# Kernel optimization log

Hardware: AMD Instinct MI355X
Metric: run time of the kernel (lower is better)

Reference implementation:

```python
import jax, jax.numpy as jnp
import numpy as np
import math

NUM_LEAD = 12
PATCHES = 100  # patch_num_v * patch_num_h = 5 * 20
HEADS = 12
HID = 768
DH = HID // HEADS  # 64
SEQ = NUM_LEAD * PATCHES + NUM_LEAD + 1  # 1213
INTER = 3072
BATCH = 8


def _layer_norm(x, g, b, eps=1e-12):
    u = x.mean(-1, keepdims=True)
    s = ((x - u) ** 2).mean(-1, keepdims=True)
    return g * (x - u) / jnp.sqrt(s + eps) + b


def _lead_mask():
    # make_mask with fusion == 0: additive bias applied to query rows [0, NUM_LEAD+1)
    cols = jnp.arange(SEQ)
    # CLS row: 1 at lead-token positions 1..NUM_LEAD
    cls_row = jnp.where((cols >= 1) & (cols < NUM_LEAD + 1), 1.0, 0.0)
    # Lead rows: 1 everywhere except own patch block
    i = jnp.arange(NUM_LEAD)[:, None]
    start = NUM_LEAD + 1 + PATCHES * i
    in_block = (cols[None, :] >= start) & (cols[None, :] < start + PATCHES)
    lead_rows = jnp.where(in_block, 0.0, 1.0)
    mask = jnp.concatenate([cls_row[None, :], lead_rows], axis=0)  # [NUM_LEAD+1, SEQ]
    return mask * (-99999.0)


def setup_inputs() -> dict:
    key = jax.random.key(0)
    ks = jax.random.split(key, 12)
    std = 0.02
    d = {
        "hidden_states": jax.random.normal(ks[0], (BATCH, SEQ, HID), jnp.float32),
        "attention_mask": jnp.zeros((BATCH, 1, 1, SEQ), jnp.float32),
        "Wq": jax.random.normal(ks[1], (HID, HID), jnp.float32) * std,
        "bq": jnp.zeros((HID,), jnp.float32),
        "Wk": jax.random.normal(ks[2], (HID, HID), jnp.float32) * std,
        "bk": jnp.zeros((HID,), jnp.float32),
        "Wv": jax.random.normal(ks[3], (HID, HID), jnp.float32) * std,
        "bv": jnp.zeros((HID,), jnp.float32),
        "Wo": jax.random.normal(ks[4], (HID, HID), jnp.float32) * std,
        "bo": jnp.zeros((HID,), jnp.float32),
        "gamma1": jnp.ones((HID,), jnp.float32),
        "beta1": jnp.zeros((HID,), jnp.float32),
        "Wi": jax.random.normal(ks[5], (HID, INTER), jnp.float32) * std,
        "bi": jnp.zeros((INTER,), jnp.float32),
        "Wd": jax.random.normal(ks[6], (INTER, HID), jnp.float32) * std,
        "bd": jnp.zeros((HID,), jnp.float32),
        "gamma2": jnp.ones((HID,), jnp.float32),
        "beta2": jnp.zeros((HID,), jnp.float32),
    }
    return d


def reference(hidden_states, attention_mask, Wq, bq, Wk, bk, Wv, bv, Wo, bo,
              gamma1, beta1, Wi, bi, Wd, bd, gamma2, beta2):
    B, S, _ = hidden_states.shape

    def heads(x):  # [B,S,HID] -> [B,H,S,DH]
        return x.reshape(B, S, HEADS, DH).transpose(0, 2, 1, 3)

    q = heads(hidden_states @ Wq + bq)
    k = heads(hidden_states @ Wk + bk)
    v = heads(hidden_states @ Wv + bv)

    scores = jnp.einsum("bhqd,bhkd->bhqk", q, k) / math.sqrt(DH)
    scores = scores + attention_mask  # broadcast [B,1,1,S]
    lead_mask = _lead_mask()  # [NUM_LEAD+1, SEQ]
    scores = scores.at[:, :, : NUM_LEAD + 1, :].add(lead_mask[None, None])

    probs = jax.nn.softmax(scores, axis=-1)  # dropout is identity in eval
    ctx = jnp.einsum("bhqk,bhkd->bhqd", probs, v)
    ctx = ctx.transpose(0, 2, 1, 3).reshape(B, S, HID)

    attn_out = _layer_norm(ctx @ Wo + bo + hidden_states, gamma1, beta1)
    inter = jax.nn.gelu(attn_out @ Wi + bi, approximate=False)  # exact erf gelu
    out = _layer_norm(inter @ Wd + bd + attn_out, gamma2, beta2)
    return out
```

## Files before the change

kernel.cpp:

```cpp
#include <hip/hip_runtime.h>
#include <hip/hip_bf16.h>
#include <stdint.h>

typedef unsigned short u16;
typedef unsigned int u32;
typedef __attribute__((ext_vector_type(8))) short frag8;
typedef __attribute__((ext_vector_type(4))) float f32x4;

#define SEQ 1213
#define SEQP 1216
#define BATCH 8
#define HEADS 12
#define DH 64
#define HID 768
#define INTER 3072
#define BS (BATCH*SEQ)
#define LOG2E 1.44269504088896f

#define MFMA(a,b,c) __builtin_amdgcn_mfma_f32_16x16x32_bf16(a,b,c,0,0,0)

__device__ __forceinline__ float b2f(u16 u){ u32 i=((u32)u)<<16; float f; __builtin_memcpy(&f,&i,4); return f; }
__device__ __forceinline__ u16 f2b(float f){ u32 i; __builtin_memcpy(&i,&f,4); i = i + 0x7fffu + ((i>>16)&1u); return (u16)(i>>16); }

__device__ __forceinline__ void async16(const u16* g, u16* l){
  __builtin_amdgcn_global_load_lds((const __attribute__((address_space(1))) u32*)(uintptr_t)g,
                                   (__attribute__((address_space(3))) u32*)(uintptr_t)l, 16, 0, 0);
}

__device__ __forceinline__ int xcd_swz(int f, int nwg){
  int cpx = nwg >> 3;
  return (f & 7)*cpx + (f >> 3);
}

__device__ __forceinline__ float gelu_exact_fast(float v){
  float y = v * 0.70710678118654752f;
  float a = fabsf(y);
  float t = __builtin_amdgcn_rcpf(fmaf(0.3275911f, a, 1.0f));
  float p = t*fmaf(t, fmaf(t, fmaf(t, fmaf(t, 1.061405429f, -1.453152027f),
                                   1.421413741f), -0.284496736f), 0.254829592f);
  float e = exp2f(a*a * -LOG2E);
  float er = fmaf(-p, e, 1.0f);
  er = copysignf(er, y);
  return 0.5f * v * (1.0f + er);
}

__global__ __launch_bounds__(256) void convert_arr(const void* __restrict__ src,
  u16* __restrict__ dst, int n8, const u16* __restrict__ probe)
{
  const bool f32 = (probe[0] == 0);
  int i = blockIdx.x*256 + threadIdx.x;
  if (i >= n8) return;
  u16 tmp[8];
  if (f32){
    const float* s = (const float*)src + (size_t)i*8;
#pragma unroll
    for (int j=0;j<8;j++) tmp[j] = f2b(s[j]);
  } else {
    *(uint4*)tmp = *((const uint4*)src + i);
  }
  *((uint4*)dst + i) = *(const uint4*)tmp;
}

__global__ __launch_bounds__(256) void convert_small(
  const void* bq, const void* bk, const void* bv, const void* bo,
  const void* bi, const void* bd, const void* g1, const void* be1,
  const void* g2, const void* be2, const void* am,
  u16* __restrict__ dst, const u16* __restrict__ probe)
{
  const int starts[12] = {0,768,1536,2304,3072,6144,6912,7680,8448,9216,9984,19688};
  const void* srcs[11] = {bq,bk,bv,bo,bi,bd,g1,be1,g2,be2,am};
  const bool f32 = (probe[0] == 0);
  int e = (blockIdx.x*256 + threadIdx.x) * 8;
  if (e >= 19688) return;
  int seg = 0;
#pragma unroll
  for (int k=1;k<11;k++) if (starts[k] <= e) seg = k;
  int off = e - starts[seg];
  const void* s = srcs[seg];
  u16 tmp[8];
  if (f32){
    const float* sf = (const float*)s + off;
#pragma unroll
    for (int j=0;j<8;j++) tmp[j] = f2b(sf[j]);
  } else {
    const u16* sh = (const u16*)s + off;
#pragma unroll
    for (int j=0;j<8;j++) tmp[j] = sh[j];
  }
  *(uint4*)(dst + e) = *(const uint4*)tmp;
}

__global__ __launch_bounds__(256) void transpose2(const void* __restrict__ in,
  u16* __restrict__ out, int R, int C, const u16* __restrict__ probe)
{
  const bool f32 = (probe[0] == 0);
  __shared__ u16 tile[32][33];
  const int bx = blockIdx.x*32, by = blockIdx.y*32;
  const int tx = threadIdx.x & 31, ty = threadIdx.x >> 5;
  if (f32){
    const float* inf_ = (const float*)in;
#pragma unroll
    for (int i=ty;i<32;i+=8) tile[i][tx] = f2b(inf_[(size_t)(by+i)*C + bx+tx]);
  } else {
    const u16* inh = (const u16*)in;
#pragma unroll
    for (int i=ty;i<32;i+=8) tile[i][tx] = inh[(size_t)(by+i)*C + bx+tx];
  }
  __syncthreads();
#pragma unroll
  for (int i=ty;i<32;i+=8) out[(size_t)(bx+i)*R + by+tx] = tile[tx][i];
}

__global__ __launch_bounds__(256) void transpose4(const void* __restrict__ w0,
  const void* __restrict__ w1, const void* __restrict__ w2, const void* __restrict__ w3,
  u16* __restrict__ dqkv, u16* __restrict__ dwo, const u16* __restrict__ probe)
{
  const bool f32 = (probe[0] == 0);
  __shared__ u16 tile[32][33];
  const int z = blockIdx.z;
  const void* in = z==0 ? w0 : (z==1 ? w1 : (z==2 ? w2 : w3));
  u16* out = (z<3) ? (dqkv + (size_t)z*768*768) : dwo;
  const int bx = blockIdx.x*32, by = blockIdx.y*32;
  const int tx = threadIdx.x & 31, ty = threadIdx.x >> 5;
  if (f32){
    const float* inf_ = (const float*)in;
#pragma unroll
    for (int i=ty;i<32;i+=8) tile[i][tx] = f2b(inf_[(size_t)(by+i)*768 + bx+tx]);
  } else {
    const u16* inh = (const u16*)in;
#pragma unroll
    for (int i=ty;i<32;i+=8) tile[i][tx] = inh[(size_t)(by+i)*768 + bx+tx];
  }
  __syncthreads();
#pragma unroll
  for (int i=ty;i<32;i+=8) out[(size_t)(bx+i)*768 + by+tx] = tile[tx][i];
}

__global__ __launch_bounds__(256) void vtrans(const u16* __restrict__ V, u16* __restrict__ VT)
{
  __shared__ u16 tile[32][33];
  const int bh = blockIdx.z;
  const int s0 = blockIdx.x*32;
  const int d0 = blockIdx.y*32;
  const int tx = threadIdx.x & 31, ty = threadIdx.x >> 5;
  const u16* Vp = V + (size_t)bh*SEQ*64;
  u16* Tp = VT + (size_t)bh*64*SEQP;
#pragma unroll
  for (int i=ty;i<32;i+=8){
    int s = s0 + i;
    tile[i][tx] = (s < SEQ) ? Vp[(size_t)s*64 + d0 + tx] : (u16)0;
  }
  __syncthreads();
#pragma unroll
  for (int i=ty;i<32;i+=8)
    Tp[(size_t)(d0 + i)*SEQP + s0 + tx] = tile[tx][i];
}

__device__ __forceinline__ void gemm_tile(
    const u16* __restrict__ A, const u16* __restrict__ BT,
    int M, int K, int m0, int n0,
    u16* ldsA, u16* ldsB, f32x4 acc[4][4])
{
  const int t = threadIdx.x;
  const int w = t >> 6, l = t & 63;
  const int lw = l & 15, lh = l >> 4;
  const int rowo = (w >> 1) << 6;
  const int colo = (w & 1) << 6;
  const int srow = w*8 + (l>>3);
  const int scol = ((l&7) ^ ((l>>3)&7)) * 8;

  const u16* gpA[4]; const u16* gpB[4];
  u16* lpA[4]; u16* lpB[4];
#pragma unroll
  for (int p=0;p<4;p++){
    int ra = m0 + p*32 + srow; if (ra >= M) ra = M-1;
    gpA[p] = A  + (size_t)ra*K + scol;
    gpB[p] = BT + (size_t)(n0 + p*32 + srow)*K + scol;
    lpA[p] = ldsA + (p*32 + w*8)*64 + l*8;
    lpB[p] = ldsB + (p*32 + w*8)*64 + l*8;
  }

  const int slot0 = lw & 7;
  for (int k0 = 0; k0 < K; k0 += 64) {
    __syncthreads();
#pragma unroll
    for (int p=0;p<4;p++) async16(gpA[p] + k0, lpA[p]);
#pragma unroll
    for (int p=0;p<4;p++) async16(gpB[p] + k0, lpB[p]);
    __syncthreads();
#pragma unroll
    for (int kk=0;kk<2;kk++){
      const int slot = ((kk*4 + lh) ^ slot0) * 8;
      frag8 af[4], bf[4];
#pragma unroll
      for (int mi=0;mi<4;mi++) af[mi] = *(const frag8*)(ldsA + (rowo + mi*16 + lw)*64 + slot);
#pragma unroll
      for (int ni=0;ni<4;ni++) bf[ni] = *(const frag8*)(ldsB + (colo + ni*16 + lw)*64 + slot);
#pragma unroll
      for (int mi=0;mi<4;mi++)
#pragma unroll
        for (int ni=0;ni<4;ni++)
          acc[mi][ni] = MFMA(af[mi], bf[ni], acc[mi][ni]);
    }
  }
}

__global__ __launch_bounds__(256,2) void gemm_qkv(
  const u16* __restrict__ A, const u16* __restrict__ BT,
  const u16* __restrict__ bq, const u16* __restrict__ bk, const u16* __restrict__ bv,
  u16* __restrict__ Qo, u16* __restrict__ Ko, u16* __restrict__ Vo)
{
  __shared__ __align__(16) u16 ldsA[128*64];
  __shared__ __align__(16) u16 ldsB[128*64];
  f32x4 acc[4][4];
#pragma unroll
  for (int i=0;i<4;i++)
#pragma unroll
    for (int j=0;j<4;j++) acc[i][j] = 0.f;
  const int m0 = blockIdx.x*128, n0 = blockIdx.y*128;
  gemm_tile(A, BT, BS, HID, m0, n0, ldsA, ldsB, acc);
  const int t=threadIdx.x, w=t>>6, l=t&63, lw=l&15, lh=l>>4;
  const int rowb = m0 + ((w>>1)<<6), colb = n0 + ((w&1)<<6);
#pragma unroll
  for (int ni=0;ni<4;ni++){
    int cc = colb + ni*16 + lw;
    int which = cc / HID;
    int n2 = cc - which*HID;
    int h = n2 >> 6, d = n2 & 63;
    const u16* bp = which==0 ? bq : (which==1 ? bk : bv);
    u16* op = which==0 ? Qo : (which==1 ? Ko : Vo);
    float bias = b2f(bp[n2]);
    float scale = which==0 ? 0.125f : 1.0f;
#pragma unroll
    for (int mi=0;mi<4;mi++){
#pragma unroll
      for (int r=0;r<4;r++){
        int rr = rowb + mi*16 + lh*4 + r;
        if (rr < BS){
          int bi_ = rr / SEQ;
          int si  = rr - bi_*SEQ;
          float v = (acc[mi][ni][r] + bias) * scale;
          op[(((size_t)(bi_*HEADS + h))*SEQ + si)*64 + d] = f2b(v);
        }
      }
    }
  }
}

__global__ __launch_bounds__(256,2) void gemm_resid(
  const u16* __restrict__ A, const u16* __restrict__ BT,
  const u16* __restrict__ bias, const u16* __restrict__ resid,
  u16* __restrict__ out, int N, int K)
{
  __shared__ __align__(16) u16 ldsA[128*64];
  __shared__ __align__(16) u16 ldsB[128*64];
  f32x4 acc[4][4];
#pragma unroll
  for (int i=0;i<4;i++)
#pragma unroll
    for (int j=0;j<4;j++) acc[i][j] = 0.f;
  const int m0 = blockIdx.x*128, n0 = blockIdx.y*128;
  gemm_tile(A, BT, BS, K, m0, n0, ldsA, ldsB, acc);
  const int t=threadIdx.x, w=t>>6, l=t&63, lw=l&15, lh=l>>4;
  const int rowb = m0 + ((w>>1)<<6), colb = n0 + ((w&1)<<6);
#pragma unroll
  for (int ni=0;ni<4;ni++){
    int cc = colb + ni*16 + lw;
    float bv_ = b2f(bias[cc]);
#pragma unroll
    for (int mi=0;mi<4;mi++){
#pragma unroll
      for (int r=0;r<4;r++){
        int rr = rowb + mi*16 + lh*4 + r;
        if (rr < BS){
          float v = acc[mi][ni][r] + bv_ + b2f(resid[(size_t)rr*N + cc]);
          out[(size_t)rr*N + cc] = f2b(v);
        }
      }
    }
  }
}

__global__ __launch_bounds__(256,2) void gemm_gelu(
  const u16* __restrict__ A, const u16* __restrict__ BT,
  const u16* __restrict__ bias, u16* __restrict__ out, int N, int K)
{
  __shared__ __align__(16) u16 ldsA[128*64];
  __shared__ __align__(16) u16 ldsB[128*64];
  f32x4 acc[4][4];
#pragma unroll
  for (int i=0;i<4;i++)
#pragma unroll
    for (int j=0;j<4;j++) acc[i][j] = 0.f;
  const int m0 = blockIdx.x*128, n0 = blockIdx.y*128;
  gemm_tile(A, BT, BS, K, m0, n0, ldsA, ldsB, acc);
  const int t=threadIdx.x, w=t>>6, l=t&63, lw=l&15, lh=l>>4;
  const int rowb = m0 + ((w>>1)<<6), colb = n0 + ((w&1)<<6);
#pragma unroll
  for (int ni=0;ni<4;ni++){
    int cc = colb + ni*16 + lw;
    float bv_ = b2f(bias[cc]);
#pragma unroll
    for (int mi=0;mi<4;mi++){
#pragma unroll
      for (int r=0;r<4;r++){
        int rr = rowb + mi*16 + lh*4 + r;
        if (rr < BS){
          float v = gelu_exact_fast(acc[mi][ni][r] + bv_);
          out[(size_t)rr*N + cc] = f2b(v);
        }
      }
    }
  }
}

__global__ __launch_bounds__(512,1) void attn_kernel(
  const u16* __restrict__ Qb, const u16* __restrict__ Kb, const u16* __restrict__ Vt,
  const u16* __restrict__ amask, u16* __restrict__ ctx)
{
  __shared__ __align__(16) u16 smem[17664];
  u16* sKb = smem;
  u16* sVb = smem + 2*64*72;
  float* sEmb = (float*)(smem + 2*64*72 + 2*64*64);
  u16* sQP = smem;

  const int t = threadIdx.x, w = t>>6, l = t&63, lw = l&15, lh = l>>4;
  int f = xcd_swz(blockIdx.y*gridDim.x + blockIdx.x, gridDim.x*gridDim.y);
  const int bh = f / gridDim.x, b = bh / HEADS;
  const int q0 = (f % gridDim.x) * 128;
  const size_t hb = (size_t)bh * SEQ * 64;
  const u16* Qp = Qb + hb;
  const u16* Kp = Kb + hb;
  const u16* Vp = Vt + (size_t)bh * 64 * SEQP;

  const int rr = t >> 3, c = t & 7;
  const int wsw = ((c ^ (rr&7))<<3);
  const int cc0 = (lw&7) ^ lh;

  {
#pragma unroll
    for (int i=0;i<2;i++){
      int qr = i*64 + rr;
      int s = q0 + qr; if (s > SEQ-1) s = SEQ-1;
      *(uint4*)(sQP + qr*72 + c*8) = *(const uint4*)(Qp + (size_t)s*64 + c*8);
    }
  }

  uint4 kreg, vreg; float emreg = 0.f;
  {
    kreg = *(const uint4*)(Kp + (size_t)rr*64 + c*8);
    vreg = *(const uint4*)(Vp + (size_t)rr*SEQP + c*8);
    if (t < 64) emreg = b2f(amask[b*SEQ + t]) * LOG2E;
  }
  __syncthreads();

  frag8 qa[2];
#pragma unroll
  for (int kk=0;kk<2;kk++) qa[kk] = *(const frag8*)(sQP + (w*16 + lw)*72 + kk*32 + lh*8);
  __syncthreads();

  *(uint4*)(sKb + rr*72 + c*8) = kreg;
  *(uint4*)(sVb + rr*64 + wsw) = vreg;
  if (t < 64) sEmb[t] = emreg;
  __syncthreads();

  union { u32 u[4]; frag8 f; } onesu;
  onesu.u[0]=onesu.u[1]=onesu.u[2]=onesu.u[3]=0x3F803F80u;
  const frag8 vones = onesu.f;

  f32x4 o[4]; f32x4 lO = 0.f;
#pragma unroll
  for (int i=0;i<4;i++) o[i] = 0.f;
  const bool leadwave = (q0 == 0) && (w == 0);

  const int nkt = (SEQ + 63) / 64;
  for (int kt = 0; kt < nkt; kt++) {
    const int p = kt & 1;
    const u16* sKp = sKb + p*64*72;
    const u16* sVp = sVb + p*64*64;
    const float* sEp = sEmb + p*64;
    const bool pf_next = (kt+1 < nkt);
    if (pf_next){
      int s = (kt+1)*64 + rr; if (s > SEQ-1) s = SEQ-1;
      kreg = *(const uint4*)(Kp + (size_t)s*64 + c*8);
      vreg = *(const uint4*)(Vp + (size_t)rr*SEQP + (kt+1)*64 + c*8);
      if (t < 64){
        int sg = (kt+1)*64 + t;
        emreg = (sg < SEQ) ? b2f(amask[b*SEQ + sg]) * LOG2E : -1e30f;
      }
    }

    f32x4 st[4];
#pragma unroll
    for (int si=0;si<4;si++){
      f32x4 a0 = 0.f;
#pragma unroll
      for (int kk=0;kk<2;kk++){
        frag8 kf = *(const frag8*)(sKp + (si*16 + lw)*72 + kk*32 + lh*8);
        a0 = MFMA(kf, qa[kk], a0);
      }
      st[si] = a0;
    }

#pragma unroll
    for (int si=0;si<4;si++){
      f32x4 emv = *(const f32x4*)(sEp + si*16 + lh*4);
#pragma unroll
      for (int r=0;r<4;r++)
        st[si][r] = exp2f(fmaf(st[si][r], LOG2E, emv[r]));
    }
    if (leadwave){
#pragma unroll
      for (int si=0;si<4;si++){
#pragma unroll
        for (int r=0;r<4;r++){
          int sg = kt*64 + si*16 + lh*4 + r;
          int q = lw;
          float pv = st[si][r];
          if (q == 0){
            if (sg >= 1 && sg < 13) pv = 0.f;
          } else if (q < 13){
            int stt = 13 + 100*(q-1);
            if (!(sg >= stt && sg < stt+100)) pv = 0.f;
          }
          st[si][r] = pv;
        }
      }
    }

    u32 pa[4], pb[4];
#pragma unroll
    for (int si=0;si<4;si++){
      asm("v_cvt_pk_bf16_f32 %0, %1, %2" : "=v"(pa[si]) : "v"(st[si][0]), "v"(st[si][1]));
      asm("v_cvt_pk_bf16_f32 %0, %1, %2" : "=v"(pb[si]) : "v"(st[si][2]), "v"(st[si][3]));
    }
    asm("v_permlane32_swap_b32 %0, %1" : "+v"(pa[0]), "+v"(pa[1]));
    asm("v_permlane32_swap_b32 %0, %1" : "+v"(pa[2]), "+v"(pa[3]));
    asm("v_permlane32_swap_b32 %0, %1" : "+v"(pb[0]), "+v"(pb[1]));
    asm("v_permlane32_swap_b32 %0, %1" : "+v"(pb[2]), "+v"(pb[3]));
    asm("v_permlane16_swap_b32 %0, %1" : "+v"(pa[0]), "+v"(pa[1]));
    asm("v_permlane16_swap_b32 %0, %1" : "+v"(pa[2]), "+v"(pa[3]));
    asm("v_permlane16_swap_b32 %0, %1" : "+v"(pb[0]), "+v"(pb[1]));
    asm("v_permlane16_swap_b32 %0, %1" : "+v"(pb[2]), "+v"(pb[3]));

#pragma unroll
    for (int kk=0;kk<2;kk++){
      union { u32 u[4]; frag8 f; } pfu;
      pfu.u[0] = pa[kk*2+0]; pfu.u[1] = pb[kk*2+0];
      pfu.u[2] = pa[kk*2+1]; pfu.u[3] = pb[kk*2+1];
      frag8 pf = pfu.f;
#pragma unroll
      for (int ni=0;ni<4;ni++){
        frag8 vf = *(const frag8*)(sVp + (ni*16+lw)*64 + ((cc0 ^ (kk<<2))<<3));
        o[ni] = MFMA(pf, vf, o[ni]);
      }
      lO = MFMA(pf, vones, lO);
    }

    if (pf_next){
      const int pn = p ^ 1;
      *(uint4*)(sKb + pn*64*72 + rr*72 + c*8) = kreg;
      *(uint4*)(sVb + pn*64*64 + rr*64 + wsw) = vreg;
      if (t < 64) sEmb[pn*64 + t] = emreg;
      __syncthreads();
    }
  }

  const int h = bh % HEADS;
#pragma unroll
  for (int r=0;r<4;r++){
    int qg = q0 + w*16 + lh*4 + r;
    if (qg < SEQ){
      float inv = 1.0f / lO[r];
#pragma unroll
      for (int ni=0;ni<4;ni++){
        ctx[((size_t)(b*SEQ) + qg)*HID + h*64 + ni*16 + lw] = f2b(o[ni][r] * inv);
      }
    }
  }
}

__global__ __launch_bounds__(256) void ln_kernel(const u16* __restrict__ y,
  const u16* __restrict__ g, const u16* __restrict__ be,
  u16* __restrict__ outb, float* __restrict__ outf)
{
  const int row = blockIdx.x, t = threadIdx.x;
  const u16* yp = y + (size_t)row*HID;
  float x0 = b2f(yp[t]), x1 = b2f(yp[t+256]), x2 = b2f(yp[t+512]);
  float s = x0 + x1 + x2;
  float q = fmaf(x0,x0, fmaf(x1,x1, x2*x2));
  __shared__ float redS[4], redQ[4];
#pragma unroll
  for (int off=1; off<64; off<<=1){
    s += __shfl_xor(s, off);
    q += __shfl_xor(q, off);
  }
  if ((t & 63) == 0){ redS[t>>6] = s; redQ[t>>6] = q; }
  __syncthreads();
  float u  = (redS[0]+redS[1]+redS[2]+redS[3]) * (1.0f/768.0f);
  float eq = (redQ[0]+redQ[1]+redQ[2]+redQ[3]) * (1.0f/768.0f);
  float var = fmaf(-u, u, eq);
  float rstd = rsqrtf(var + 1e-12f);
  float d0=x0-u, d1=x1-u, d2=x2-u;
  float v0 = b2f(g[t])    *(d0*rstd) + b2f(be[t]);
  float v1 = b2f(g[t+256])*(d1*rstd) + b2f(be[t+256]);
  float v2 = b2f(g[t+512])*(d2*rstd) + b2f(be[t+512]);
  if (outf){
    float* op = outf + (size_t)row*HID;
    op[t] = v0; op[t+256] = v1; op[t+512] = v2;
  } else {
    u16* op = outb + (size_t)row*HID;
    op[t] = f2b(v0); op[t+256] = f2b(v1); op[t+512] = f2b(v2);
  }
}

extern "C" void kernel_launch(void* const* d_in, const int* in_sizes, int n_in,
                              void* d_out, int out_size, void* d_ws, size_t ws_size,
                              hipStream_t stream)
{
  const void* hidden = d_in[0];
  const void* amask  = d_in[1];
  const void* Wq = d_in[2];  const void* bq = d_in[3];
  const void* Wk = d_in[4];  const void* bk = d_in[5];
  const void* Wv = d_in[6];  const void* bv = d_in[7];
  const void* Wo = d_in[8];  const void* bo = d_in[9];
  const void* g1 = d_in[10]; const void* be1= d_in[11];
  const void* Wi = d_in[12]; const void* bi = d_in[13];
  const void* Wd = d_in[14]; const void* bd = d_in[15];
  const void* g2 = d_in[16]; const void* be2= d_in[17];
  const u16* probe = (const u16*)g1;

  char* ws = (char*)d_ws;
  size_t off = 0;
  auto alloc = [&](size_t elems)->u16* {
    u16* p = (u16*)(ws + off);
    off += ((elems*2 + 255) & ~(size_t)255);
    return p;
  };
  u16* hiddenC = alloc((size_t)BS*HID);
  u16* smallC  = alloc((size_t)19688);
  u16* WqkvT = alloc((size_t)2304*768);
  u16* WoT   = alloc((size_t)768*768);
  u16* WiT   = alloc((size_t)3072*768);
  u16* WdT   = alloc((size_t)768*3072);
  u16* Qb    = alloc((size_t)BS*HID);
  u16* Kb    = alloc((size_t)BS*HID);
  u16* VTb   = alloc((size_t)BS*HID);
  u16* y1    = alloc((size_t)BS*HID);
  u16* interb = Qb;
  u16* ctxb  = alloc((size_t)BS*HID);
  u16* attn_out = alloc((size_t)BS*HID);
  u16* y2 = ctxb;
  u16* Vb = ctxb;

  const u16* c_bq = smallC;        const u16* c_bk = smallC+768;
  const u16* c_bv = smallC+1536;   const u16* c_bo = smallC+2304;
  const u16* c_bi = smallC+3072;   const u16* c_bd = smallC+6144;
  const u16* c_g1 = smallC+6912;   const u16* c_be1= smallC+7680;
  const u16* c_g2 = smallC+8448;   const u16* c_be2= smallC+9216;
  const u16* c_am = smallC+9984;

  dim3 blk(256);
  convert_arr<<<dim3((BS*HID/8 + 255)/256), blk, 0, stream>>>(hidden, hiddenC, BS*HID/8, probe);
  convert_small<<<dim3(10), blk, 0, stream>>>(bq,bk,bv,bo,bi,bd,g1,be1,g2,be2,amask, smallC, probe);
  transpose4<<<dim3(24,24,4),blk,0,stream>>>(Wq, Wk, Wv, Wo, WqkvT, WoT, probe);
  transpose2<<<dim3(96,24),blk,0,stream>>>(Wi, WiT, 768, 3072, probe);
  transpose2<<<dim3(24,96),blk,0,stream>>>(Wd, WdT, 3072, 768, probe);

  gemm_qkv<<<dim3(76,18),blk,0,stream>>>(hiddenC, WqkvT, c_bq,c_bk,c_bv, Qb,Kb,Vb);
  vtrans<<<dim3(38,2,96),blk,0,stream>>>(Vb, VTb);
  attn_kernel<<<dim3(10,96),dim3(512),0,stream>>>(Qb,Kb,VTb, c_am, ctxb);
  gemm_resid<<<dim3(76,6),blk,0,stream>>>(ctxb, WoT, c_bo, hiddenC, y1, 768, 768);
  ln_kernel<<<dim3(BS),blk,0,stream>>>(y1, c_g1, c_be1, attn_out, nullptr);
  gemm_gelu<<<dim3(76,24),blk,0,stream>>>(attn_out, WiT, c_bi, interb, 3072, 768);
  gemm_resid<<<dim3(76,6),blk,0,stream>>>(interb, WdT, c_bd, attn_out, y2, 768, 3072);
  ln_kernel<<<dim3(BS),blk,0,stream>>>(y2, c_g2, c_be2, nullptr, (float*)d_out);
}
```

Measured before the change: 493.4 us.

## Double-buffer LDS tiles in GEMM mainloop to overlap loads with MFMA

Converts the shared GEMM tile loop from a load-sync-compute pattern to a two-stage LDS double buffer. The next K-slice is prefetched with async global-to-LDS copies while MFMAs run on the current buffer, and one barrier per iteration replaces two. This aims to hide global memory latency in the QKV, output-projection and FFN GEMMs. It doubles LDS use per block to 64KB, which may reduce occupancy relative to the launch_bounds(256,2) target.

```diff
diff --git a/kernel.cpp b/kernel.cpp
--- a/kernel.cpp
+++ b/kernel.cpp
@@ -170,38 +170,50 @@
   const int scol = ((l&7) ^ ((l>>3)&7)) * 8;
 
   const u16* gpA[4]; const u16* gpB[4];
-  u16* lpA[4]; u16* lpB[4];
+  int lofs[4];
 #pragma unroll
   for (int p=0;p<4;p++){
     int ra = m0 + p*32 + srow; if (ra >= M) ra = M-1;
     gpA[p] = A  + (size_t)ra*K + scol;
     gpB[p] = BT + (size_t)(n0 + p*32 + srow)*K + scol;
-    lpA[p] = ldsA + (p*32 + w*8)*64 + l*8;
-    lpB[p] = ldsB + (p*32 + w*8)*64 + l*8;
-  }
+    lofs[p] = (p*32 + w*8)*64 + l*8;
+  }
+
+#pragma unroll
+  for (int p=0;p<4;p++) async16(gpA[p], ldsA + lofs[p]);
+#pragma unroll
+  for (int p=0;p<4;p++) async16(gpB[p], ldsB + lofs[p]);
 
   const int slot0 = lw & 7;
+  int buf = 0;
   for (int k0 = 0; k0 < K; k0 += 64) {
+    asm volatile("s_waitcnt vmcnt(0)" ::: "memory");
     __syncthreads();
-#pragma unroll
-    for (int p=0;p<4;p++) async16(gpA[p] + k0, lpA[p]);
-#pragma unroll
-    for (int p=0;p<4;p++) async16(gpB[p] + k0, lpB[p]);
-    __syncthreads();
+    const int nbuf = buf ^ 1;
+    if (k0 + 64 < K){
+      const int no = nbuf*(128*64);
+#pragma unroll
+      for (int p=0;p<4;p++) async16(gpA[p] + k0 + 64, ldsA + no + lofs[p]);
+#pragma unroll
+      for (int p=0;p<4;p++) async16(gpB[p] + k0 + 64, ldsB + no + lofs[p]);
+    }
+    const u16* lA = ldsA + buf*(128*64);
+    const u16* lB = ldsB + buf*(128*64);
 #pragma unroll
     for (int kk=0;kk<2;kk++){
       const int slot = ((kk*4 + lh) ^ slot0) * 8;
       frag8 af[4], bf[4];
 #pragma unroll
-      for (int mi=0;mi<4;mi++) af[mi] = *(const frag8*)(ldsA + (rowo + mi*16 + lw)*64 + slot);
-#pragma unroll
-      for (int ni=0;ni<4;ni++) bf[ni] = *(const frag8*)(ldsB + (colo + ni*16 + lw)*64 + slot);
+      for (int mi=0;mi<4;mi++) af[mi] = *(const frag8*)(lA + (rowo + mi*16 + lw)*64 + slot);
+#pragma unroll
+      for (int ni=0;ni<4;ni++) bf[ni] = *(const frag8*)(lB + (colo + ni*16 + lw)*64 + slot);
 #pragma unroll
       for (int mi=0;mi<4;mi++)
 #pragma unroll
         for (int ni=0;ni<4;ni++)
           acc[mi][ni] = MFMA(af[mi], bf[ni], acc[mi][ni]);
     }
+    buf = nbuf;
   }
 }
 
@@ -210,8 +222,8 @@
   const u16* __restrict__ bq, const u16* __restrict__ bk, const u16* __restrict__ bv,
   u16* __restrict__ Qo, u16* __restrict__ Ko, u16* __restrict__ Vo)
 {
-  __shared__ __align__(16) u16 ldsA[128*64];
-  __shared__ __align__(16) u16 ldsB[128*64];
+  __shared__ __align__(16) u16 ldsA[2*128*64];
+  __shared__ __align__(16) u16 ldsB[2*128*64];
   f32x4 acc[4][4];
 #pragma unroll
   for (int i=0;i<4;i++)
@@ -252,8 +264,8 @@
   const u16* __restrict__ bias, const u16* __restrict__ resid,
   u16* __restrict__ out, int N, int K)
 {
-  __shared__ __align__(16) u16 ldsA[128*64];
-  __shared__ __align__(16) u16 ldsB[128*64];
+  __shared__ __align__(16) u16 ldsA[2*128*64];
+  __shared__ __align__(16) u16 ldsB[2*128*64];
   f32x4 acc[4][4];
 #pragma unroll
   for (int i=0;i<4;i++)
@@ -285,8 +297,8 @@
   const u16* __restrict__ A, const u16* __restrict__ BT,
   const u16* __restrict__ bias, u16* __restrict__ out, int N, int K)
 {
-  __shared__ __align__(16) u16 ldsA[128*64];
-  __shared__ __align__(16) u16 ldsB[128*64];
+  __shared__ __align__(16) u16 ldsA[2*128*64];
+  __shared__ __align__(16) u16 ldsB[2*128*64];
   f32x4 acc[4][4];
 #pragma unroll
   for (int i=0;i<4;i++)
```

New measurement: 481.9 us. -2.3%, faster.
